# Performance work log

Hardware: AMD Instinct MI355X
Metric: run time of the kernel (lower is better)

The kernel has to match this reference:

```python
import jax, jax.numpy as jnp
import numpy as np

B = 1024
E = 512
NUM_HEADS = 8
EPS = 1e-5  # torch LayerNorm default


def _mha(x, w_qkv, b_qkv, w_o, b_o):
    """torch nn.MultiheadAttention (batch_first, self-attn, no dropout).
    x: [N, S, E]; w_qkv: [3E, E]; w_o: [E, E]."""
    N, S, Ex = x.shape
    H = NUM_HEADS
    D = Ex // H
    qkv = x @ w_qkv.T + b_qkv                      # [N, S, 3E]
    q, k, v = jnp.split(qkv, 3, axis=-1)
    q = q.reshape(N, S, H, D).transpose(0, 2, 1, 3)  # [N, H, S, D]
    k = k.reshape(N, S, H, D).transpose(0, 2, 1, 3)
    v = v.reshape(N, S, H, D).transpose(0, 2, 1, 3)
    scores = jnp.einsum('nhqd,nhkd->nhqk', q, k) * (D ** -0.5)
    attn = jax.nn.softmax(scores, axis=-1)
    out = jnp.einsum('nhqk,nhkd->nhqd', attn, v)
    out = out.transpose(0, 2, 1, 3).reshape(N, S, Ex)
    return out @ w_o.T + b_o


def _box_perm(g):
    """Permute 9x9 grid so each 3x3 box becomes a contiguous row of 9.
    This permutation is its own inverse. g: [B, 9, 9, E]."""
    Bx = g.shape[0]
    return (g.reshape(Bx, 3, 3, 3, 3, E)
             .transpose(0, 1, 3, 2, 4, 5)
             .reshape(Bx, 9, 9, E))


def setup_inputs() -> dict:
    key = jax.random.key(0)
    ks = jax.random.split(key, 16)
    s = 0.02
    inp = {'x': jax.random.normal(ks[0], (B, 81, E), jnp.float32)}
    for i, p in enumerate(['row', 'col', 'box']):
        inp[p + '_wqkv'] = jax.random.normal(ks[1 + 2 * i], (3 * E, E), jnp.float32) * s
        inp[p + '_bqkv'] = jnp.zeros((3 * E,), jnp.float32)
        inp[p + '_wo'] = jax.random.normal(ks[2 + 2 * i], (E, E), jnp.float32) * s
        inp[p + '_bo'] = jnp.zeros((E,), jnp.float32)
    inp['w1'] = jax.random.normal(ks[7], (2 * E, 3 * E), jnp.float32) * s
    inp['b1'] = jnp.zeros((2 * E,), jnp.float32)
    inp['w2'] = jax.random.normal(ks[8], (E, 2 * E), jnp.float32) * s
    inp['b2'] = jnp.zeros((E,), jnp.float32)
    inp['gamma'] = jnp.ones((E,), jnp.float32)
    inp['beta'] = jnp.zeros((E,), jnp.float32)
    return inp


def reference(x, row_wqkv, row_bqkv, row_wo, row_bo,
              col_wqkv, col_bqkv, col_wo, col_bo,
              box_wqkv, box_bqkv, box_wo, box_bo,
              w1, b1, w2, b2, gamma, beta):
    Bx = x.shape[0]
    # Row attention: rows are already contiguous groups of 9.
    row_out = _mha(x.reshape(Bx * 9, 9, E), row_wqkv, row_bqkv, row_wo, row_bo)
    row_out = row_out.reshape(Bx, 81, E)
    # Column attention: transpose grid so columns are contiguous.
    col_x = x.reshape(Bx, 9, 9, E).transpose(0, 2, 1, 3).reshape(Bx * 9, 9, E)
    col_out = _mha(col_x, col_wqkv, col_bqkv, col_wo, col_bo)
    col_out = col_out.reshape(Bx, 9, 9, E).transpose(0, 2, 1, 3).reshape(Bx, 81, E)
    # Box attention: permute grid so each 3x3 box is contiguous.
    box_x = _box_perm(x.reshape(Bx, 9, 9, E)).reshape(Bx * 9, 9, E)
    box_out = _mha(box_x, box_wqkv, box_bqkv, box_wo, box_bo)
    box_out = _box_perm(box_out.reshape(Bx, 9, 9, E)).reshape(Bx, 81, E)
    # Constraint mixer MLP.
    combined = jnp.concatenate([row_out, col_out, box_out], axis=-1)  # [B,81,3E]
    h = jax.nn.gelu(combined @ w1.T + b1, approximate=False)
    mixed = h @ w2.T + b2
    # Residual + LayerNorm.
    y = x + mixed
    mu = jnp.mean(y, axis=-1, keepdims=True)
    var = jnp.var(y, axis=-1, keepdims=True)
    return (y - mu) * jax.lax.rsqrt(var + EPS) * gamma + beta
```

## Files before the change

### kernel.cpp

```cpp
#include <hip/hip_runtime.h>
#include <hip/hip_bf16.h>
#include <math.h>

typedef __hip_bfloat16 bf16;
typedef __attribute__((ext_vector_type(8))) short s8v;
typedef __attribute__((ext_vector_type(4))) short s4v;
typedef __attribute__((ext_vector_type(4))) float f4v;

static __device__ __forceinline__ float bfs2f(short s) {
    return __uint_as_float(((unsigned)(unsigned short)s) << 16);
}
static __device__ __forceinline__ short f2bfs(float f) {
    __hip_bfloat16 h = __float2bfloat16(f);
    return *reinterpret_cast<short*>(&h);
}

__global__ __launch_bounds__(256)
void cvt_f32_bf16(const float* __restrict__ in, bf16* __restrict__ out, long n4)
{
    const long i = (long)blockIdx.x * 256 + threadIdx.x;
    if (i >= n4) return;
    const float4 v = reinterpret_cast<const float4*>(in)[i];
    s4v o;
    o[0] = f2bfs(v.x); o[1] = f2bfs(v.y); o[2] = f2bfs(v.z); o[3] = f2bfs(v.w);
    reinterpret_cast<s4v*>(out)[i] = o;
}

__global__ __launch_bounds__(256)
void cvt_t_f32_bf16(const float* __restrict__ in, bf16* __restrict__ out,
                    int R, int C)
{
    __shared__ float t[32][33];
    const int bx = blockIdx.x * 32;
    const int by = blockIdx.y * 32;
    const int tx = threadIdx.x & 31;
    const int ty = threadIdx.x >> 5;
#pragma unroll
    for (int r = ty; r < 32; r += 8)
        t[r][tx] = in[(long)(by + r) * C + bx + tx];
    __syncthreads();
#pragma unroll
    for (int r = ty; r < 32; r += 8)
        out[(long)(bx + r) * R + by + tx] = __float2bfloat16(t[tx][r]);
}

__global__ __launch_bounds__(256)
void fold_b1(const float* __restrict__ w1, const float* __restrict__ bo0,
             const float* __restrict__ bo1, const float* __restrict__ bo2,
             const float* __restrict__ b1, float* __restrict__ b1p)
{
    const int m = blockIdx.x * 256 + threadIdx.x;
    float s = b1[m];
    const float* w = w1 + (long)m * 1536;
    for (int k = 0; k < 512; ++k) s += w[k]        * bo0[k];
    for (int k = 0; k < 512; ++k) s += w[512 + k]  * bo1[k];
    for (int k = 0; k < 512; ++k) s += w[1024 + k] * bo2[k];
    b1p[m] = s;
}

template<int ACT>
__global__ __launch_bounds__(256)
void gemm_bt(const bf16* __restrict__ A, const bf16* __restrict__ B,
             const float* __restrict__ bias, bf16* __restrict__ C,
             int K, int lda, int ldc, int coff)
{
    __shared__ __align__(16) bf16 sA[128 * 64];
    __shared__ __align__(16) bf16 sB[128 * 64];
    const int tid  = threadIdx.x;
    const int lane = tid & 63;
    const int nwg = gridDim.x * gridDim.y;
    const int bid = blockIdx.x + gridDim.x * blockIdx.y;
    const int sbid = (bid & 7) * (nwg >> 3) + (bid >> 3);
    const int bCol = sbid % gridDim.x;
    const int bRow = sbid / gridDim.x;
    const int wr = ((tid >> 7) & 1) * 64;
    const int wc = ((tid >> 6) & 1) * 64;

    f4v acc[4][4];
#pragma unroll
    for (int i = 0; i < 4; ++i)
#pragma unroll
        for (int j = 0; j < 4; ++j) acc[i][j] = (f4v)(0.0f);

    const int srow = tid >> 3;
    const int scol = ((tid & 7) ^ (srow & 7)) * 8;
    const bf16* Ab = A + (long)(bRow * 128 + srow) * lda + scol;
    const bf16* Bb = B + (long)(bCol * 128 + srow) * K + scol;
    char* sAc = (char*)sA;
    char* sBc = (char*)sB;
    const int dst = tid * 16;

    const int fr = lane & 15;
    const int hi = lane >> 4;
    const int rx = fr & 7;

    const int nk = K >> 6;
    for (int kt = 0; kt < nk; ++kt) {
        const int k0 = kt << 6;
        __syncthreads();
#pragma unroll
        for (int p = 0; p < 4; ++p) {
            __builtin_amdgcn_global_load_lds(
                (const __attribute__((address_space(1))) unsigned int*)(Ab + (long)(p * 32) * lda + k0),
                (__attribute__((address_space(3))) unsigned int*)(sAc + p * 4096 + dst),
                16, 0, 0);
            __builtin_amdgcn_global_load_lds(
                (const __attribute__((address_space(1))) unsigned int*)(Bb + (long)(p * 32) * K + k0),
                (__attribute__((address_space(3))) unsigned int*)(sBc + p * 4096 + dst),
                16, 0, 0);
        }
        __syncthreads();
#pragma unroll
        for (int s = 0; s < 2; ++s) {
            const int co = ((s * 4 + hi) ^ rx) * 8;
            s8v af[4], bfr[4];
#pragma unroll
            for (int mi = 0; mi < 4; ++mi)
                af[mi] = *(const s8v*)(&sA[(wr + mi * 16 + fr) * 64 + co]);
#pragma unroll
            for (int ni = 0; ni < 4; ++ni)
                bfr[ni] = *(const s8v*)(&sB[(wc + ni * 16 + fr) * 64 + co]);
#pragma unroll
            for (int mi = 0; mi < 4; ++mi)
#pragma unroll
                for (int ni = 0; ni < 4; ++ni)
                    acc[mi][ni] = __builtin_amdgcn_mfma_f32_16x16x32_bf16(
                        af[mi], bfr[ni], acc[mi][ni], 0, 0, 0);
        }
    }

    const int frow = hi * 4;
    const long rowBase = (long)bRow * 128 + wr;
    const int  colBase = bCol * 128 + wc;
#pragma unroll
    for (int ni = 0; ni < 4; ++ni) {
        const int col = colBase + ni * 16 + fr;
        const float bi = bias ? bias[coff + col] : 0.0f;
#pragma unroll
        for (int mi = 0; mi < 4; ++mi) {
#pragma unroll
            for (int j = 0; j < 4; ++j) {
                float v = acc[mi][ni][j] + bi;
                if (ACT == 1) {
                    const float u = v * (0.7978845608f + 0.0356774081f * v * v);
                    const float t = 1.0f - 2.0f / (__expf(2.0f * u) + 1.0f);
                    v = 0.5f * v * (1.0f + t);
                }
                const long r = rowBase + mi * 16 + frow + j;
                C[r * (long)ldc + coff + col] = __float2bfloat16(v);
            }
        }
    }
}

__global__ __launch_bounds__(256)
void attn9(const bf16* __restrict__ qkv, bf16* __restrict__ outg,
           long chunk_base)
{
    __shared__ __align__(16) bf16 sQKV[9 * 1536];
    __shared__ float sP[8 * 81];
    __shared__ int sTok[9];
    const int tid = threadIdx.x;
    const int branch = blockIdx.y;
    const int bx = blockIdx.x;
    const int s = (bx & 7) * (2304 >> 3) + (bx >> 3);
    const int b = s / 9, g = s % 9;

    if (tid < 9) {
        const int p = tid;
        int cell;
        if (branch == 0)      cell = g * 9 + p;
        else if (branch == 1) cell = p * 9 + g;
        else                  cell = ((g / 3) * 3 + p / 3) * 9 + (g % 3) * 3 + (p % 3);
        sTok[p] = b * 81 + cell;
    }
    __syncthreads();

    const long brOff = (long)branch * 1536;
    for (int c = tid; c < 1728; c += 256) {
        const int p = c / 192;
        const int off = (c - p * 192) * 8;
        *(s8v*)(&sQKV[p * 1536 + off]) =
            *(const s8v*)(&qkv[(long)sTok[p] * 4608 + brOff + off]);
    }
    __syncthreads();

    for (int t = tid; t < 648; t += 256) {
        const int h = t / 81;
        const int r = t - h * 81;
        const int i = r / 9, j = r - (r / 9) * 9;
        const bf16* q = &sQKV[i * 1536 + h * 64];
        const bf16* k = &sQKV[j * 1536 + 512 + h * 64];
        float accd = 0.0f;
#pragma unroll
        for (int dc = 0; dc < 8; ++dc) {
            s8v qv = *(const s8v*)(q + dc * 8);
            s8v kv = *(const s8v*)(k + dc * 8);
#pragma unroll
            for (int e2 = 0; e2 < 8; ++e2)
                accd += bfs2f(qv[e2]) * bfs2f(kv[e2]);
        }
        sP[t] = accd * 0.125f;
    }
    __syncthreads();

    if (tid < 72) {
        float* row = &sP[tid * 9];
        float m = row[0];
#pragma unroll
        for (int j = 1; j < 9; ++j) m = fmaxf(m, row[j]);
        float sum = 0.f, e[9];
#pragma unroll
        for (int j = 0; j < 9; ++j) { e[j] = expf(row[j] - m); sum += e[j]; }
        const float inv = 1.0f / sum;
#pragma unroll
        for (int j = 0; j < 9; ++j) row[j] = e[j] * inv;
    }
    __syncthreads();

    for (int t = tid; t < 576; t += 256) {
        const int i = t >> 6;
        const int c8 = (t & 63) * 8;
        const int h = (t & 63) >> 3;
        const float* prow = &sP[h * 81 + i * 9];
        float accv[8];
#pragma unroll
        for (int q2 = 0; q2 < 8; ++q2) accv[q2] = 0.f;
#pragma unroll
        for (int j = 0; j < 9; ++j) {
            const float p = prow[j];
            s8v vv = *(const s8v*)(&sQKV[j * 1536 + 1024 + c8]);
#pragma unroll
            for (int q2 = 0; q2 < 8; ++q2)
                accv[q2] += p * bfs2f(vv[q2]);
        }
        s8v ov;
#pragma unroll
        for (int q2 = 0; q2 < 8; ++q2) ov[q2] = f2bfs(accv[q2]);
        *(s8v*)(&outg[(chunk_base + sTok[i]) * 1536 + branch * 512 + c8]) = ov;
    }
}

__global__ __launch_bounds__(256)
void ln_res(const float* __restrict__ x, const bf16* __restrict__ mixed,
            const float* __restrict__ gamma, const float* __restrict__ beta,
            float* __restrict__ out)
{
    const int tid = threadIdx.x;
    const int lane = tid & 63;
    const long row = (long)blockIdx.x * 4 + (tid >> 6);
    const long base = row * 512 + lane * 8;
    const float4 x0 = *(const float4*)(&x[base]);
    const float4 x1 = *(const float4*)(&x[base + 4]);
    const s8v mv = *(const s8v*)(&mixed[base]);
    float y[8];
    y[0] = x0.x + bfs2f(mv[0]); y[1] = x0.y + bfs2f(mv[1]);
    y[2] = x0.z + bfs2f(mv[2]); y[3] = x0.w + bfs2f(mv[3]);
    y[4] = x1.x + bfs2f(mv[4]); y[5] = x1.y + bfs2f(mv[5]);
    y[6] = x1.z + bfs2f(mv[6]); y[7] = x1.w + bfs2f(mv[7]);
    float sum = 0.f, sq = 0.f;
#pragma unroll
    for (int j = 0; j < 8; ++j) { sum += y[j]; sq += y[j] * y[j]; }
#pragma unroll
    for (int o = 32; o > 0; o >>= 1) {
        sum += __shfl_xor(sum, o, 64);
        sq  += __shfl_xor(sq, o, 64);
    }
    const float mean = sum * (1.f / 512.f);
    const float inv = rsqrtf(sq * (1.f / 512.f) - mean * mean + 1e-5f);
    const float4 g0 = *(const float4*)(&gamma[lane * 8]);
    const float4 g1 = *(const float4*)(&gamma[lane * 8 + 4]);
    const float4 b0 = *(const float4*)(&beta[lane * 8]);
    const float4 b1 = *(const float4*)(&beta[lane * 8 + 4]);
    float4 o0, o1;
    o0.x = (y[0] - mean) * inv * g0.x + b0.x;
    o0.y = (y[1] - mean) * inv * g0.y + b0.y;
    o0.z = (y[2] - mean) * inv * g0.z + b0.z;
    o0.w = (y[3] - mean) * inv * g0.w + b0.w;
    o1.x = (y[4] - mean) * inv * g1.x + b1.x;
    o1.y = (y[5] - mean) * inv * g1.y + b1.y;
    o1.z = (y[6] - mean) * inv * g1.z + b1.z;
    o1.w = (y[7] - mean) * inv * g1.w + b1.w;
    *(float4*)(&out[base]) = o0;
    *(float4*)(&out[base + 4]) = o1;
}

extern "C" void kernel_launch(void* const* d_in, const int* in_sizes, int n_in,
                              void* d_out, int out_size, void* d_ws, size_t ws_size,
                              hipStream_t stream)
{
    (void)in_sizes; (void)n_in; (void)out_size; (void)ws_size;
    const float* x     = (const float*)d_in[0];
    const float* w1f   = (const float*)d_in[13];
    const float* b1f   = (const float*)d_in[14];
    const float* b2f   = (const float*)d_in[16];
    const float* gamma = (const float*)d_in[17];
    const float* beta  = (const float*)d_in[18];

    char* ws = (char*)d_ws;
    bf16* attnall   = (bf16*)(ws);
    bf16* mixed     = (bf16*)(ws);
    char* R         = ws + 254803968LL;
    bf16* qkv3chunk = (bf16*)(R);
    bf16* xb        = (bf16*)(R + 191102976LL);
    bf16* h         = (bf16*)(R);
    char* wb        = ws + 530841600LL;
    long off = 0;
    bf16* wqkv3_b = (bf16*)(wb + off); off += 4718592;
    bf16* woT_b[3];
    for (int i = 0; i < 3; ++i) { woT_b[i] = (bf16*)(wb + off); off += 524288; }
    bf16* w1_b  = (bf16*)(wb + off); off += 3145728;
    bf16* w2_b  = (bf16*)(wb + off); off += 1048576;
    bf16* Wp    = (bf16*)(wb + off); off += 3145728;
    float* b1p  = (float*)(wb + off); off += 4096;
    float* bqkv3 = (float*)(wb + off); off += 18432;

    const dim3 blk(256, 1, 1);

    cvt_f32_bf16<<<dim3(41472), blk, 0, stream>>>(x, xb, 10616832L);
    for (int i = 0; i < 3; ++i) {
        cvt_f32_bf16<<<dim3(768), blk, 0, stream>>>(
            (const float*)d_in[1 + i * 4], wqkv3_b + (long)i * 786432, 196608L);
        cvt_t_f32_bf16<<<dim3(16, 16), blk, 0, stream>>>(
            (const float*)d_in[3 + i * 4], woT_b[i], 512, 512);
        hipMemcpyAsync(bqkv3 + i * 1536, d_in[2 + i * 4], 1536 * sizeof(float),
                       hipMemcpyDeviceToDevice, stream);
    }
    cvt_f32_bf16<<<dim3(1536), blk, 0, stream>>>(w1f, w1_b, 393216L);
    cvt_f32_bf16<<<dim3(512), blk, 0, stream>>>((const float*)d_in[15], w2_b, 131072L);

    fold_b1<<<dim3(4), blk, 0, stream>>>(w1f, (const float*)d_in[4],
                                         (const float*)d_in[8], (const float*)d_in[12],
                                         b1f, b1p);

    for (int br = 0; br < 3; ++br)
        gemm_bt<0><<<dim3(4, 8), blk, 0, stream>>>(
            w1_b + br * 512, woT_b[br], nullptr, Wp, 512, 1536, 1536, br * 512);

    const long ROWS_C = 20736;
    for (int c = 0; c < 4; ++c) {
        const bf16* xA = xb + c * ROWS_C * 512;
        gemm_bt<0><<<dim3(36, 162), blk, 0, stream>>>(
            xA, wqkv3_b, bqkv3, qkv3chunk, 512, 512, 4608, 0);
        attn9<<<dim3(2304, 3), blk, 0, stream>>>(qkv3chunk, attnall, c * ROWS_C);
    }
    gemm_bt<1><<<dim3(8, 648), blk, 0, stream>>>(attnall, Wp, b1p, h, 1536, 1536, 1024, 0);
    gemm_bt<0><<<dim3(4, 648), blk, 0, stream>>>(h, w2_b, b2f, mixed, 1024, 1024, 512, 0);
    ln_res<<<dim3(20736), blk, 0, stream>>>(x, mixed, gamma, beta, (float*)d_out);
}
```

Baseline: 1.578 ms.

## Replace 128x128 GEMM with double-buffered 256x256 tile, 512-thread pipelined kernel

Replaces the 128x128, 256-thread GEMM with a 256x256 tile kernel run by 8 waves. It double-buffers A and B in LDS and prefetches the next K tiles with global_load_lds, interleaved with the MFMA phases. Manual s_waitcnt, s_barrier, sched_barrier and s_setprio calls are used to overlap global loads with compute and to raise data reuse per tile. The cost is about 128KB of LDS per block and much more delicate synchronisation, so occupancy drops to one block per CU. All four GEMM launch configurations are resized to the larger tiles.

```diff
diff --git a/kernel.cpp b/kernel.cpp
--- a/kernel.cpp
+++ b/kernel.cpp
@@ -59,95 +59,141 @@
 }
 
 template<int ACT>
-__global__ __launch_bounds__(256)
-void gemm_bt(const bf16* __restrict__ A, const bf16* __restrict__ B,
+__global__ __launch_bounds__(512, 2)
+void gemm256(const bf16* __restrict__ A, const bf16* __restrict__ B,
              const float* __restrict__ bias, bf16* __restrict__ C,
              int K, int lda, int ldc, int coff)
 {
-    __shared__ __align__(16) bf16 sA[128 * 64];
-    __shared__ __align__(16) bf16 sB[128 * 64];
+    __shared__ __align__(16) bf16 sA[2][256 * 64];
+    __shared__ __align__(16) bf16 sB[2][256 * 64];
     const int tid  = threadIdx.x;
     const int lane = tid & 63;
-    const int nwg = gridDim.x * gridDim.y;
-    const int bid = blockIdx.x + gridDim.x * blockIdx.y;
-    const int sbid = (bid & 7) * (nwg >> 3) + (bid >> 3);
-    const int bCol = sbid % gridDim.x;
-    const int bRow = sbid / gridDim.x;
-    const int wr = ((tid >> 7) & 1) * 64;
-    const int wc = ((tid >> 6) & 1) * 64;
-
-    f4v acc[4][4];
-#pragma unroll
-    for (int i = 0; i < 4; ++i)
+    const int wid  = tid >> 6;
+    const int nwg  = gridDim.x * gridDim.y;
+    const int orig = blockIdx.x + gridDim.x * blockIdx.y;
+    const int q = nwg >> 3, r = nwg & 7, xcd = orig & 7;
+    const int sb = (xcd < r ? xcd * (q + 1) : r * (q + 1) + (xcd - r) * q) + (orig >> 3);
+    const int bCol = sb % gridDim.x;
+    const int bRow = sb / gridDim.x;
+
+    const int wr  = (wid >> 2) * 128;
+    const int wc  = (wid & 3) * 64;
+    const int fr  = lane & 15;
+    const int hi4 = lane >> 4;
+    const int rx  = fr & 7;
+
+    f4v acc[8][4];
+#pragma unroll
+    for (int i = 0; i < 8; ++i)
 #pragma unroll
         for (int j = 0; j < 4; ++j) acc[i][j] = (f4v)(0.0f);
 
     const int srow = tid >> 3;
     const int scol = ((tid & 7) ^ (srow & 7)) * 8;
-    const bf16* Ab = A + (long)(bRow * 128 + srow) * lda + scol;
-    const bf16* Bb = B + (long)(bCol * 128 + srow) * K + scol;
-    char* sAc = (char*)sA;
-    char* sBc = (char*)sB;
-    const int dst = tid * 16;
-
-    const int fr = lane & 15;
-    const int hi = lane >> 4;
-    const int rx = fr & 7;
+    const bf16* Abase = A + (long)(bRow * 256 + srow) * lda + scol;
+    const bf16* Bbase = B + (long)(bCol * 256 + srow) * K + scol;
+
+#define GL16(src, dst)                                                          \
+    __builtin_amdgcn_global_load_lds(                                           \
+        (const __attribute__((address_space(1))) unsigned int*)(src),           \
+        (__attribute__((address_space(3))) unsigned int*)(dst), 16, 0, 0)
+
+#define STAGE_A(h, tt, bc) do {                                                 \
+    const bf16* g_ = Abase + (long)(h) * 128 * lda + (long)(tt) * 64;           \
+    char* d_ = (char*)sA[bc] + (h) * 16384 + tid * 16;                          \
+    GL16(g_, d_); GL16(g_ + 64 * (long)lda, d_ + 8192); } while (0)
+
+#define STAGE_B(h, tt, bc) do {                                                 \
+    const bf16* g_ = Bbase + (long)(h) * 128 * K + (long)(tt) * 64;             \
+    char* d_ = (char*)sB[bc] + (h) * 16384 + tid * 16;                          \
+    GL16(g_, d_); GL16(g_ + 64 * (long)K, d_ + 8192); } while (0)
 
     const int nk = K >> 6;
-    for (int kt = 0; kt < nk; ++kt) {
-        const int k0 = kt << 6;
-        __syncthreads();
+
+    STAGE_A(0, 0, 0); STAGE_A(1, 0, 0);
+    STAGE_B(0, 0, 0); STAGE_B(1, 0, 0);
+    STAGE_B(0, 1, 1); STAGE_B(1, 1, 1);
+    asm volatile("s_waitcnt vmcnt(4)" ::: "memory");
+    __builtin_amdgcn_s_barrier();
+    __builtin_amdgcn_sched_barrier(0);
+
+    for (int t = 0; t < nk; ++t) {
+        const int c = t & 1;
+        const char* sAc = (const char*)sA[c];
+        const char* sBc = (const char*)sB[c];
+        s8v bfr[4][2];
 #pragma unroll
         for (int p = 0; p < 4; ++p) {
-            __builtin_amdgcn_global_load_lds(
-                (const __attribute__((address_space(1))) unsigned int*)(Ab + (long)(p * 32) * lda + k0),
-                (__attribute__((address_space(3))) unsigned int*)(sAc + p * 4096 + dst),
-                16, 0, 0);
-            __builtin_amdgcn_global_load_lds(
-                (const __attribute__((address_space(1))) unsigned int*)(Bb + (long)(p * 32) * K + k0),
-                (__attribute__((address_space(3))) unsigned int*)(sBc + p * 4096 + dst),
-                16, 0, 0);
+            s8v afr[2][2];
+#pragma unroll
+            for (int m2 = 0; m2 < 2; ++m2)
+#pragma unroll
+                for (int kk = 0; kk < 2; ++kk)
+                    afr[m2][kk] = *(const s8v*)(sAc
+                        + (wr + (2 * p + m2) * 16 + fr) * 128
+                        + (((kk * 4 + hi4) ^ rx) << 4));
+            if (p == 0) {
+#pragma unroll
+                for (int ni = 0; ni < 4; ++ni)
+#pragma unroll
+                    for (int kk = 0; kk < 2; ++kk)
+                        bfr[ni][kk] = *(const s8v*)(sBc
+                            + (wc + ni * 16 + fr) * 128
+                            + (((kk * 4 + hi4) ^ rx) << 4));
+            }
+            if (p == 0 && t + 1 < nk) STAGE_A(0, t + 1, c ^ 1);
+            if (p == 1 && t + 1 < nk) STAGE_A(1, t + 1, c ^ 1);
+            if (p == 2 && t + 2 < nk) STAGE_B(0, t + 2, c);
+            if (p == 3 && t + 2 < nk) STAGE_B(1, t + 2, c);
+
+            __builtin_amdgcn_s_barrier();
+            asm volatile("s_waitcnt lgkmcnt(0)" ::: "memory");
+            __builtin_amdgcn_sched_barrier(0);
+            __builtin_amdgcn_s_setprio(1);
+#pragma unroll
+            for (int kk = 0; kk < 2; ++kk)
+#pragma unroll
+                for (int m2 = 0; m2 < 2; ++m2)
+#pragma unroll
+                    for (int ni = 0; ni < 4; ++ni)
+                        acc[2 * p + m2][ni] = __builtin_amdgcn_mfma_f32_16x16x32_bf16(
+                            afr[m2][kk], bfr[ni][kk], acc[2 * p + m2][ni], 0, 0, 0);
+            __builtin_amdgcn_s_setprio(0);
+            __builtin_amdgcn_sched_barrier(0);
+            if (p == 3) {
+                if (t + 2 < nk) {
+                    asm volatile("s_waitcnt vmcnt(4)" ::: "memory");
+                } else if (t + 1 < nk) {
+                    asm volatile("s_waitcnt vmcnt(0)" ::: "memory");
+                }
+            }
+            __builtin_amdgcn_s_barrier();
+            __builtin_amdgcn_sched_barrier(0);
         }
-        __syncthreads();
-#pragma unroll
-        for (int s = 0; s < 2; ++s) {
-            const int co = ((s * 4 + hi) ^ rx) * 8;
-            s8v af[4], bfr[4];
-#pragma unroll
-            for (int mi = 0; mi < 4; ++mi)
-                af[mi] = *(const s8v*)(&sA[(wr + mi * 16 + fr) * 64 + co]);
-#pragma unroll
-            for (int ni = 0; ni < 4; ++ni)
-                bfr[ni] = *(const s8v*)(&sB[(wc + ni * 16 + fr) * 64 + co]);
-#pragma unroll
-            for (int mi = 0; mi < 4; ++mi)
-#pragma unroll
-                for (int ni = 0; ni < 4; ++ni)
-                    acc[mi][ni] = __builtin_amdgcn_mfma_f32_16x16x32_bf16(
-                        af[mi], bfr[ni], acc[mi][ni], 0, 0, 0);
-        }
-    }
-
-    const int frow = hi * 4;
-    const long rowBase = (long)bRow * 128 + wr;
-    const int  colBase = bCol * 128 + wc;
+    }
+#undef STAGE_A
+#undef STAGE_B
+#undef GL16
+
+    const int frow = hi4 * 4;
+    const long rowBase = (long)bRow * 256 + wr;
+    const int  colBase = bCol * 256 + wc;
 #pragma unroll
     for (int ni = 0; ni < 4; ++ni) {
         const int col = colBase + ni * 16 + fr;
         const float bi = bias ? bias[coff + col] : 0.0f;
 #pragma unroll
-        for (int mi = 0; mi < 4; ++mi) {
+        for (int mi = 0; mi < 8; ++mi) {
 #pragma unroll
             for (int j = 0; j < 4; ++j) {
                 float v = acc[mi][ni][j] + bi;
                 if (ACT == 1) {
                     const float u = v * (0.7978845608f + 0.0356774081f * v * v);
-                    const float t = 1.0f - 2.0f / (__expf(2.0f * u) + 1.0f);
-                    v = 0.5f * v * (1.0f + t);
+                    const float tnh = 1.0f - 2.0f / (__expf(2.0f * u) + 1.0f);
+                    v = 0.5f * v * (1.0f + tnh);
                 }
-                const long r = rowBase + mi * 16 + frow + j;
-                C[r * (long)ldc + coff + col] = __float2bfloat16(v);
+                const long rr = rowBase + mi * 16 + frow + j;
+                C[rr * (long)ldc + coff + col] = __float2bfloat16(v);
             }
         }
     }
@@ -189,13 +235,13 @@
         const int h = t / 81;
         const int r = t - h * 81;
         const int i = r / 9, j = r - (r / 9) * 9;
-        const bf16* q = &sQKV[i * 1536 + h * 64];
-        const bf16* k = &sQKV[j * 1536 + 512 + h * 64];
+        const bf16* qp = &sQKV[i * 1536 + h * 64];
+        const bf16* kp = &sQKV[j * 1536 + 512 + h * 64];
         float accd = 0.0f;
 #pragma unroll
         for (int dc = 0; dc < 8; ++dc) {
-            s8v qv = *(const s8v*)(q + dc * 8);
-            s8v kv = *(const s8v*)(k + dc * 8);
+            s8v qv = *(const s8v*)(qp + dc * 8);
+            s8v kv = *(const s8v*)(kp + dc * 8);
 #pragma unroll
             for (int e2 = 0; e2 < 8; ++e2)
                 accd += bfs2f(qv[e2]) * bfs2f(kv[e2]);
@@ -316,6 +362,7 @@
     float* bqkv3 = (float*)(wb + off); off += 18432;
 
     const dim3 blk(256, 1, 1);
+    const dim3 blk512(512, 1, 1);
 
     cvt_f32_bf16<<<dim3(41472), blk, 0, stream>>>(x, xb, 10616832L);
     for (int i = 0; i < 3; ++i) {
@@ -334,17 +381,17 @@
                                          b1f, b1p);
 
     for (int br = 0; br < 3; ++br)
-        gemm_bt<0><<<dim3(4, 8), blk, 0, stream>>>(
+        gemm256<0><<<dim3(2, 4), blk512, 0, stream>>>(
             w1_b + br * 512, woT_b[br], nullptr, Wp, 512, 1536, 1536, br * 512);
 
     const long ROWS_C = 20736;
     for (int c = 0; c < 4; ++c) {
         const bf16* xA = xb + c * ROWS_C * 512;
-        gemm_bt<0><<<dim3(36, 162), blk, 0, stream>>>(
+        gemm256<0><<<dim3(18, 81), blk512, 0, stream>>>(
             xA, wqkv3_b, bqkv3, qkv3chunk, 512, 512, 4608, 0);
         attn9<<<dim3(2304, 3), blk, 0, stream>>>(qkv3chunk, attnall, c * ROWS_C);
     }
-    gemm_bt<1><<<dim3(8, 648), blk, 0, stream>>>(attnall, Wp, b1p, h, 1536, 1536, 1024, 0);
-    gemm_bt<0><<<dim3(4, 648), blk, 0, stream>>>(h, w2_b, b2f, mixed, 1024, 1024, 512, 0);
+    gemm256<1><<<dim3(4, 324), blk512, 0, stream>>>(attnall, Wp, b1p, h, 1536, 1536, 1024, 0);
+    gemm256<0><<<dim3(2, 324), blk512, 0, stream>>>(h, w2_b, b2f, mixed, 1024, 1024, 512, 0);
     ln_res<<<dim3(20736), blk, 0, stream>>>(x, mixed, gamma, beta, (float*)d_out);
 }
```

After: 1.727 ms. +9.4%, slower.
